# Kernel tuning notes

Hardware: AMD Instinct MI355X
Metric: run time of the kernel (lower is better)

The kernel has to match this reference:

```python
import jax, jax.numpy as jnp
import numpy as np

N_NODES = 100000
D_IN = 128
D_OUT = 128
N_EDGES = 1600000
BN_EPS = 1e-5
LEAKY_SLOPE = 0.01


def setup_inputs() -> dict:
    key = jax.random.key(0)
    ks = jax.random.split(key, 8)
    x = jax.random.normal(ks[0], (N_NODES, D_IN), dtype=jnp.float32)
    edge_index = jax.random.randint(ks[1], (2, N_EDGES), 0, N_NODES, dtype=jnp.int32)
    scale = 1.0 / np.sqrt(D_IN)
    W = jax.random.uniform(ks[2], (D_IN, D_OUT), jnp.float32, -scale, scale)
    b = jax.random.uniform(ks[3], (D_OUT,), jnp.float32, -scale, scale)
    bn_gamma = jnp.ones((D_IN,), jnp.float32)
    bn_beta = jnp.zeros((D_IN,), jnp.float32)
    bn_mean = jax.random.normal(ks[4], (D_IN,), jnp.float32) * 0.01
    bn_var = jax.random.uniform(ks[5], (D_IN,), jnp.float32, 0.5, 1.5)
    rs_W = jax.random.uniform(ks[6], (D_IN, D_OUT), jnp.float32, -scale, scale)
    rs_b = jax.random.uniform(ks[7], (D_OUT,), jnp.float32, -scale, scale)
    return {"x": x, "edge_index": edge_index, "W": W, "b": b,
            "bn_gamma": bn_gamma, "bn_beta": bn_beta,
            "bn_mean": bn_mean, "bn_var": bn_var,
            "rs_W": rs_W, "rs_b": rs_b}


def reference(x, edge_index, W, b, bn_gamma, bn_beta, bn_mean, bn_var, rs_W, rs_b):
    N = x.shape[0]
    # F.normalize: row-wise L2 normalization (eps=1e-12)
    nrm = jnp.sqrt(jnp.sum(x * x, axis=1, keepdims=True))
    x = x / jnp.maximum(nrm, 1e-12)
    # BatchNorm1d (eval mode, running stats)
    x = (x - bn_mean) * jax.lax.rsqrt(bn_var + BN_EPS) * bn_gamma + bn_beta
    # GCNConv: add self-loops, symmetric normalization
    loops = jnp.arange(N, dtype=edge_index.dtype)
    src = jnp.concatenate([edge_index[0], loops])  # [E+N] source j
    dst = jnp.concatenate([edge_index[1], loops])  # [E+N] target i
    deg = jax.ops.segment_sum(jnp.ones(dst.shape, x.dtype), dst, num_segments=N)
    dinv = jax.lax.rsqrt(deg)  # self-loops guarantee deg >= 1
    norm = dinv[src] * dinv[dst]  # [E+N]
    xw = x @ W  # [N, D_OUT]
    msgs = xw[src] * norm[:, None]  # [E+N, D_OUT] gather
    out = jax.ops.segment_sum(msgs, dst, num_segments=N) + b  # scatter-add
    # residual linear on the normalized+BN'd input
    out = out + x @ rs_W + rs_b
    # LeakyReLU (dropout is identity in eval mode)
    return jnp.where(out >= 0, out, LEAKY_SLOPE * out)
```

## Files before the change

kernel.cpp:

```cpp
#include <hip/hip_runtime.h>
#include <hip/hip_fp16.h>


#define NN 100000
#define DD 128
#define EE 1600000
#define BN_EPS 1e-5f
#define SLOPE 0.01f

#define NBKT 98
#define BWID 1024
#define CAPP 20480
#define EPB  4096
#define EBLK 391

struct __align__(8) H4 { __half2 a, b; };

typedef _Float16 f16x8 __attribute__((ext_vector_type(8)));
typedef float    f32x4 __attribute__((ext_vector_type(4)));

__global__ __launch_bounds__(256) void k_binA(const int* __restrict__ src,
                                              const int* __restrict__ dst,
                                              int* __restrict__ gcur,
                                              int* __restrict__ pairs,
                                              const float* __restrict__ W,
                                              const float* __restrict__ rsW,
                                              const float* __restrict__ b,
                                              const float* __restrict__ rb,
                                              __half* __restrict__ WhT,
                                              float* __restrict__ bias2) {
  int t = threadIdx.x;
  if (blockIdx.x >= EBLK) {
    int blk = blockIdx.x - EBLK;
    if (blk == 128) {
      if (t < DD) bias2[t] = b[t] + rb[t];
    } else {
      float v = (t < 128) ? W[t * 128 + blk] : rsW[(t - 128) * 128 + blk];
      WhT[blk * 256 + t] = __float2half(v);
    }
    return;
  }
  __shared__ int hist[2][NBKT];
  __shared__ int cur[2][NBKT];
  int w2 = (t >> 6) & 1;
  if (t < NBKT) { hist[0][t] = 0; hist[1][t] = 0; }
  __syncthreads();
  int e0 = blockIdx.x * EPB;
  #pragma unroll 4
  for (int i = 0; i < EPB / 256; ++i) {
    int e = e0 + i * 256 + t;
    if (e < EE) atomicAdd(&hist[w2][dst[e] >> 10], 1);
  }
  __syncthreads();
  if (t < NBKT) {
    int h0 = hist[0][t], h1 = hist[1][t];
    int b0 = atomicAdd(&gcur[t], h0 + h1);
    cur[0][t] = b0;
    cur[1][t] = b0 + h0;
  }
  __syncthreads();
  #pragma unroll 4
  for (int i = 0; i < EPB / 256; ++i) {
    int e = e0 + i * 256 + t;
    if (e < EE) {
      int d = dst[e], s = src[e];
      int bk = d >> 10;
      int r = atomicAdd(&cur[w2][bk], 1);
      pairs[(size_t)bk * CAPP + r] = ((d & 1023) << 17) | s;
    }
  }
}

__global__ __launch_bounds__(1024) void k_binB(const int* __restrict__ gcur,
                                               const int* __restrict__ pairs,
                                               int* __restrict__ csr,
                                               int2* __restrict__ startdeg,
                                               float* __restrict__ dinv) {
  __shared__ int hist[BWID];
  __shared__ int excl[BWID];
  __shared__ int wsum[16];
  int b = blockIdx.x, t = threadIdx.x;
  hist[t] = 0;
  __syncthreads();
  int pbase = b * CAPP;
  int cnt = gcur[b];
  for (int i = t; i < cnt; i += BWID)
    atomicAdd(&hist[pairs[pbase + i] >> 17], 1);
  __syncthreads();
  int v = hist[t];
  int lane = t & 63, w = t >> 6;
  int incl = v;
  #pragma unroll
  for (int off = 1; off < 64; off <<= 1) {
    int n = __shfl_up(incl, off, 64);
    if (lane >= off) incl += n;
  }
  if (lane == 63) wsum[w] = incl;
  __syncthreads();
  if (t < 16) {
    int orig = wsum[t];
    int s = orig;
    #pragma unroll
    for (int off = 1; off < 16; off <<= 1) {
      int n = __shfl_up(s, off, 64);
      if (t >= off) s += n;
    }
    wsum[t] = s - orig;
  }
  __syncthreads();
  int myexcl = (incl - v) + wsum[w];
  excl[t] = myexcl;
  int node = b * BWID + t;
  if (node < NN) {
    dinv[node] = rsqrtf((float)(v + 1));
    startdeg[node] = make_int2(pbase + myexcl, v);
  }
  __syncthreads();
  for (int i = t; i < cnt; i += BWID) {
    int p = pairs[pbase + i];
    int pos = atomicAdd(&excl[p >> 17], 1);
    csr[pbase + pos] = p & 0x1FFFF;
  }
}

__global__ void k_norm_bn(const float* __restrict__ x,
                          const float* __restrict__ gamma,
                          const float* __restrict__ beta,
                          const float* __restrict__ mean,
                          const float* __restrict__ var,
                          const float* __restrict__ dinv,
                          __half* __restrict__ Ah, __half* __restrict__ zp) {
  int row = blockIdx.x * 4 + (threadIdx.x >> 6);
  int lane = threadIdx.x & 63;
  if (row >= NN) return;
  float2 v = ((const float2*)(x + (size_t)row * DD))[lane];
  float ss = v.x * v.x + v.y * v.y;
  #pragma unroll
  for (int off = 32; off > 0; off >>= 1) ss += __shfl_xor(ss, off);
  float s = 1.0f / fmaxf(sqrtf(ss), 1e-12f);
  float di = dinv[row];
  int c = lane * 2;
  float g0 = gamma[c]     * rsqrtf(var[c]     + BN_EPS);
  float g1 = gamma[c + 1] * rsqrtf(var[c + 1] + BN_EPS);
  float ox = (v.x * s - mean[c])     * g0 + beta[c];
  float oy = (v.y * s - mean[c + 1]) * g1 + beta[c + 1];
  ((__half2*)(Ah + (size_t)row * 256 + 128))[lane] = __floats2half2_rn(ox, oy);
  ((__half2*)(zp + (size_t)row * DD))[lane] = __floats2half2_rn(di * ox, di * oy);
}

__global__ void k_aggregate(const __half* __restrict__ zp,
                            __half* __restrict__ Ah,
                            const int2* __restrict__ startdeg,
                            const int* __restrict__ csr,
                            const float* __restrict__ dinv) {
  int lane = threadIdx.x & 63;
  int half = lane >> 5;
  int l32  = lane & 31;
  int node = blockIdx.x * 8 + (threadIdx.x >> 6) * 2 + half;
  int2 sd = startdeg[node];
  int k = sd.x, end = sd.x + sd.y;
  float di = dinv[node];
  const H4* zr = (const H4*)zp;
  float4 acc = make_float4(0.f, 0.f, 0.f, 0.f);
  for (; k + 8 <= end; k += 8) {
    int j[8];
    #pragma unroll
    for (int u = 0; u < 8; ++u) j[u] = csr[k + u];
    H4 a[8];
    #pragma unroll
    for (int u = 0; u < 8; ++u) a[u] = zr[(size_t)j[u] * 32 + l32];
    #pragma unroll
    for (int u = 0; u < 8; ++u) {
      float2 fa = __half22float2(a[u].a), fb = __half22float2(a[u].b);
      acc.x += fa.x; acc.y += fa.y; acc.z += fb.x; acc.w += fb.y;
    }
  }
  if (k + 4 <= end) {
    int j[4];
    #pragma unroll
    for (int u = 0; u < 4; ++u) j[u] = csr[k + u];
    H4 a[4];
    #pragma unroll
    for (int u = 0; u < 4; ++u) a[u] = zr[(size_t)j[u] * 32 + l32];
    #pragma unroll
    for (int u = 0; u < 4; ++u) {
      float2 fa = __half22float2(a[u].a), fb = __half22float2(a[u].b);
      acc.x += fa.x; acc.y += fa.y; acc.z += fb.x; acc.w += fb.y;
    }
    k += 4;
  }
  for (; k < end; ++k) {
    int j0 = csr[k];
    H4 a0 = zr[(size_t)j0 * 32 + l32];
    float2 fa = __half22float2(a0.a), fb = __half22float2(a0.b);
    acc.x += fa.x; acc.y += fa.y; acc.z += fb.x; acc.w += fb.y;
  }
  H4 zs = zr[(size_t)node * 32 + l32];
  float2 za = __half22float2(zs.a), zb2 = __half22float2(zs.b);
  H4 o;
  o.a = __floats2half2_rn((acc.x + za.x) * di, (acc.y + za.y) * di);
  o.b = __floats2half2_rn((acc.z + zb2.x) * di, (acc.w + zb2.y) * di);
  ((H4*)Ah)[(size_t)node * 64 + l32] = o;
}

__global__ __launch_bounds__(512, 2) void k_gemm(
    const __half* __restrict__ Ah, const __half* __restrict__ WhT,
    const float* __restrict__ bias2, float* __restrict__ out) {
  __shared__ __align__(16) char Bs[65536];
  const int tid = threadIdx.x;
  const int w  = tid >> 6;
  const int l  = tid & 63;
  const int lm = l & 15;
  const int lk = l >> 4;
  const int row0 = blockIdx.x * 256 + w * 32;

  int rA0 = row0 + lm;
  int rA1 = row0 + 16 + lm;
  if (rA0 >= NN) rA0 = NN - 1;
  if (rA1 >= NN) rA1 = NN - 1;

  const __half* a0p = Ah + (size_t)rA0 * 256 + lk * 8;
  const __half* a1p = Ah + (size_t)rA1 * 256 + lk * 8;
  f16x8 a0[8], a1[8];
  #pragma unroll
  for (int ks = 0; ks < 8; ++ks) {
    a0[ks] = *(const f16x8*)(a0p + ks * 32);
    a1[ks] = *(const f16x8*)(a1p + ks * 32);
  }

  #pragma unroll
  for (int i = 0; i < 8; ++i) {
    int idx = tid + i * 512;
    int byte = idx * 16;
    int swz = byte ^ (((byte >> 9) & 7) << 4);
    *(float4*)(Bs + swz) = ((const float4*)WhT)[idx];
  }
  __syncthreads();

  f32x4 acc0[8], acc1[8];
  #pragma unroll
  for (int c = 0; c < 8; ++c) {
    acc0[c] = (f32x4)(0.f);
    acc1[c] = (f32x4)(0.f);
  }

  #pragma unroll
  for (int ks = 0; ks < 8; ++ks) {
    #pragma unroll
    for (int c = 0; c < 8; ++c) {
      int byte = (c * 16 + lm) * 512 + lk * 16 + ks * 64;
      f16x8 b = *(const f16x8*)(Bs + (byte ^ ((lm & 7) << 4)));
      acc0[c] = __builtin_amdgcn_mfma_f32_16x16x32_f16(a0[ks], b, acc0[c], 0, 0, 0);
      acc1[c] = __builtin_amdgcn_mfma_f32_16x16x32_f16(a1[ks], b, acc1[c], 0, 0, 0);
    }
  }

  int orow0 = row0 + lk * 4;
  int orow1 = row0 + 16 + lk * 4;
  #pragma unroll
  for (int c = 0; c < 8; ++c) {
    int col = c * 16 + lm;
    float bs = bias2[col];
    #pragma unroll
    for (int r = 0; r < 4; ++r) {
      int g0 = orow0 + r;
      if (g0 < NN) {
        float v = acc0[c][r] + bs;
        out[(size_t)g0 * 128 + col] = (v >= 0.f) ? v : SLOPE * v;
      }
      int g1 = orow1 + r;
      if (g1 < NN) {
        float v = acc1[c][r] + bs;
        out[(size_t)g1 * 128 + col] = (v >= 0.f) ? v : SLOPE * v;
      }
    }
  }
}

extern "C" void kernel_launch(void* const* d_in, const int* in_sizes, int n_in,
                              void* d_out, int out_size, void* d_ws, size_t ws_size,
                              hipStream_t stream) {
  const float* x     = (const float*)d_in[0];
  const int*   ei    = (const int*)d_in[1];
  const float* W     = (const float*)d_in[2];
  const float* b     = (const float*)d_in[3];
  const float* gamma = (const float*)d_in[4];
  const float* beta  = (const float*)d_in[5];
  const float* mean  = (const float*)d_in[6];
  const float* var   = (const float*)d_in[7];
  const float* rsW   = (const float*)d_in[8];
  const float* rsb   = (const float*)d_in[9];
  float* out = (float*)d_out;
  const int* src = ei;
  const int* dst = ei + EE;

  __half* Ah       = (__half*)d_ws;
  __half* zp       = Ah + (size_t)NN * 256;
  int2*   startdeg = (int2*)(zp + (size_t)NN * DD);
  float*  dinv     = (float*)(startdeg + NN);
  int*    gcur     = (int*)(dinv + NN);
  int*    pairs    = gcur + 128;
  int*    csr      = pairs + NBKT * CAPP;
  __half* WhT      = (__half*)(csr + NBKT * CAPP);
  float*  bias2    = (float*)(WhT + 128 * 256);

  hipMemsetAsync(gcur, 0, 128 * sizeof(int), stream);
  k_binA<<<EBLK + 129, 256, 0, stream>>>(src, dst, gcur, pairs,
                                         W, rsW, b, rsb, WhT, bias2);
  k_binB<<<NBKT, 1024, 0, stream>>>(gcur, pairs, csr, startdeg, dinv);
  k_norm_bn<<<NN / 4, 256, 0, stream>>>(x, gamma, beta, mean, var, dinv, Ah, zp);
  k_aggregate<<<NN / 8, 256, 0, stream>>>(zp, Ah, startdeg, csr, dinv);
  k_gemm<<<(NN + 255) / 256, 512, 0, stream>>>(Ah, WhT, bias2, out);
}
```

Before: 272.6 us.

## Stage binning through LDS, widen aggregate gathers to 16B, shrink GEMM blocks

The first binning pass now sorts each block's edges by bucket in shared memory before writing them out, so global stores become contiguous runs instead of scattered atomically-placed writes. The second pass builds the per-bucket CSR in shared memory and writes it out linearly. Aggregation uses 16 lanes per node with 16-byte f16x8 loads, so each wave handles four nodes. The GEMM drops to 256-thread blocks of 128 rows, so the shared-memory weight tile is loaded more often in total. The new LCAP clamp silently truncates any bucket with more than 18432 edges, which risks wrong results on denser inputs.

```diff
diff --git a/kernel.cpp b/kernel.cpp
--- a/kernel.cpp
+++ b/kernel.cpp
@@ -11,10 +11,9 @@
 #define NBKT 98
 #define BWID 1024
 #define CAPP 20480
+#define LCAP 18432
 #define EPB  4096
 #define EBLK 391
-
-struct __align__(8) H4 { __half2 a, b; };
 
 typedef _Float16 f16x8 __attribute__((ext_vector_type(8)));
 typedef float    f32x4 __attribute__((ext_vector_type(4)));
@@ -40,34 +39,60 @@
     }
     return;
   }
-  __shared__ int hist[2][NBKT];
-  __shared__ int cur[2][NBKT];
-  int w2 = (t >> 6) & 1;
-  if (t < NBKT) { hist[0][t] = 0; hist[1][t] = 0; }
+  __shared__ int hist[NBKT];
+  __shared__ int cur[NBKT];
+  __shared__ int gofs[NBKT];
+  __shared__ int wtot;
+  __shared__ int sortedp[EPB];
+  __shared__ unsigned char sbk[EPB];
+  if (t < NBKT) hist[t] = 0;
   __syncthreads();
   int e0 = blockIdx.x * EPB;
-  #pragma unroll 4
-  for (int i = 0; i < EPB / 256; ++i) {
+  int pr[16];
+  int bkr[16];
+  #pragma unroll
+  for (int i = 0; i < 16; ++i) {
     int e = e0 + i * 256 + t;
-    if (e < EE) atomicAdd(&hist[w2][dst[e] >> 10], 1);
-  }
-  __syncthreads();
-  if (t < NBKT) {
-    int h0 = hist[0][t], h1 = hist[1][t];
-    int b0 = atomicAdd(&gcur[t], h0 + h1);
-    cur[0][t] = b0;
-    cur[1][t] = b0 + h0;
-  }
-  __syncthreads();
-  #pragma unroll 4
-  for (int i = 0; i < EPB / 256; ++i) {
-    int e = e0 + i * 256 + t;
+    bkr[i] = -1;
     if (e < EE) {
       int d = dst[e], s = src[e];
-      int bk = d >> 10;
-      int r = atomicAdd(&cur[w2][bk], 1);
-      pairs[(size_t)bk * CAPP + r] = ((d & 1023) << 17) | s;
-    }
+      bkr[i] = d >> 10;
+      pr[i] = ((d & 1023) << 17) | s;
+      atomicAdd(&hist[bkr[i]], 1);
+    }
+  }
+  __syncthreads();
+  {
+    int v = (t < NBKT) ? hist[t] : 0;
+    int incl = v;
+    #pragma unroll
+    for (int off = 1; off < 64; off <<= 1) {
+      int n = __shfl_up(incl, off, 64);
+      if ((t & 63) >= off) incl += n;
+    }
+    if (t == 63) wtot = incl;
+    __syncthreads();
+    if (t < NBKT) {
+      int ex = incl - v + ((t >= 64) ? wtot : 0);
+      cur[t] = ex;
+      int gb = atomicAdd(&gcur[t], v);
+      gofs[t] = t * CAPP + gb - ex;
+    }
+  }
+  __syncthreads();
+  #pragma unroll
+  for (int i = 0; i < 16; ++i) {
+    if (bkr[i] >= 0) {
+      int r = atomicAdd(&cur[bkr[i]], 1);
+      sortedp[r] = pr[i];
+      sbk[r] = (unsigned char)bkr[i];
+    }
+  }
+  __syncthreads();
+  int cnt = min(EPB, EE - e0);
+  for (int i = t; i < cnt; i += 256) {
+    int bq = sbk[i];
+    pairs[gofs[bq] + i] = sortedp[i];
   }
 }
 
@@ -79,11 +104,13 @@
   __shared__ int hist[BWID];
   __shared__ int excl[BWID];
   __shared__ int wsum[16];
+  __shared__ int sortedp[LCAP];
   int b = blockIdx.x, t = threadIdx.x;
   hist[t] = 0;
   __syncthreads();
   int pbase = b * CAPP;
   int cnt = gcur[b];
+  if (cnt > LCAP) cnt = LCAP;
   for (int i = t; i < cnt; i += BWID)
     atomicAdd(&hist[pairs[pbase + i] >> 17], 1);
   __syncthreads();
@@ -119,8 +146,11 @@
   for (int i = t; i < cnt; i += BWID) {
     int p = pairs[pbase + i];
     int pos = atomicAdd(&excl[p >> 17], 1);
-    csr[pbase + pos] = p & 0x1FFFF;
-  }
+    sortedp[pos] = p & 0x1FFFF;
+  }
+  __syncthreads();
+  for (int i = t; i < cnt; i += BWID)
+    csr[pbase + i] = sortedp[i];
 }
 
 __global__ void k_norm_bn(const float* __restrict__ x,
@@ -154,56 +184,54 @@
                             const int* __restrict__ csr,
                             const float* __restrict__ dinv) {
   int lane = threadIdx.x & 63;
-  int half = lane >> 5;
-  int l32  = lane & 31;
-  int node = blockIdx.x * 8 + (threadIdx.x >> 6) * 2 + half;
+  int q   = lane >> 4;
+  int l16 = lane & 15;
+  int node = blockIdx.x * 16 + (threadIdx.x >> 6) * 4 + q;
   int2 sd = startdeg[node];
   int k = sd.x, end = sd.x + sd.y;
   float di = dinv[node];
-  const H4* zr = (const H4*)zp;
-  float4 acc = make_float4(0.f, 0.f, 0.f, 0.f);
+  const f16x8* zr = (const f16x8*)zp;
+  float acc[8] = {0.f, 0.f, 0.f, 0.f, 0.f, 0.f, 0.f, 0.f};
   for (; k + 8 <= end; k += 8) {
     int j[8];
     #pragma unroll
     for (int u = 0; u < 8; ++u) j[u] = csr[k + u];
-    H4 a[8];
-    #pragma unroll
-    for (int u = 0; u < 8; ++u) a[u] = zr[(size_t)j[u] * 32 + l32];
-    #pragma unroll
-    for (int u = 0; u < 8; ++u) {
-      float2 fa = __half22float2(a[u].a), fb = __half22float2(a[u].b);
-      acc.x += fa.x; acc.y += fa.y; acc.z += fb.x; acc.w += fb.y;
-    }
+    f16x8 a[8];
+    #pragma unroll
+    for (int u = 0; u < 8; ++u) a[u] = zr[(size_t)j[u] * 16 + l16];
+    #pragma unroll
+    for (int u = 0; u < 8; ++u)
+      #pragma unroll
+      for (int vv = 0; vv < 8; ++vv) acc[vv] += (float)a[u][vv];
   }
   if (k + 4 <= end) {
     int j[4];
     #pragma unroll
     for (int u = 0; u < 4; ++u) j[u] = csr[k + u];
-    H4 a[4];
-    #pragma unroll
-    for (int u = 0; u < 4; ++u) a[u] = zr[(size_t)j[u] * 32 + l32];
-    #pragma unroll
-    for (int u = 0; u < 4; ++u) {
-      float2 fa = __half22float2(a[u].a), fb = __half22float2(a[u].b);
-      acc.x += fa.x; acc.y += fa.y; acc.z += fb.x; acc.w += fb.y;
-    }
+    f16x8 a[4];
+    #pragma unroll
+    for (int u = 0; u < 4; ++u) a[u] = zr[(size_t)j[u] * 16 + l16];
+    #pragma unroll
+    for (int u = 0; u < 4; ++u)
+      #pragma unroll
+      for (int vv = 0; vv < 8; ++vv) acc[vv] += (float)a[u][vv];
     k += 4;
   }
   for (; k < end; ++k) {
     int j0 = csr[k];
-    H4 a0 = zr[(size_t)j0 * 32 + l32];
-    float2 fa = __half22float2(a0.a), fb = __half22float2(a0.b);
-    acc.x += fa.x; acc.y += fa.y; acc.z += fb.x; acc.w += fb.y;
-  }
-  H4 zs = zr[(size_t)node * 32 + l32];
-  float2 za = __half22float2(zs.a), zb2 = __half22float2(zs.b);
-  H4 o;
-  o.a = __floats2half2_rn((acc.x + za.x) * di, (acc.y + za.y) * di);
-  o.b = __floats2half2_rn((acc.z + zb2.x) * di, (acc.w + zb2.y) * di);
-  ((H4*)Ah)[(size_t)node * 64 + l32] = o;
-}
-
-__global__ __launch_bounds__(512, 2) void k_gemm(
+    f16x8 a0 = zr[(size_t)j0 * 16 + l16];
+    #pragma unroll
+    for (int vv = 0; vv < 8; ++vv) acc[vv] += (float)a0[vv];
+  }
+  f16x8 zs = zr[(size_t)node * 16 + l16];
+  f16x8 o;
+  #pragma unroll
+  for (int vv = 0; vv < 8; ++vv)
+    o[vv] = (_Float16)((acc[vv] + (float)zs[vv]) * di);
+  ((f16x8*)Ah)[(size_t)node * 32 + l16] = o;
+}
+
+__global__ __launch_bounds__(256) void k_gemm(
     const __half* __restrict__ Ah, const __half* __restrict__ WhT,
     const float* __restrict__ bias2, float* __restrict__ out) {
   __shared__ __align__(16) char Bs[65536];
@@ -212,7 +240,7 @@
   const int l  = tid & 63;
   const int lm = l & 15;
   const int lk = l >> 4;
-  const int row0 = blockIdx.x * 256 + w * 32;
+  const int row0 = blockIdx.x * 128 + w * 32;
 
   int rA0 = row0 + lm;
   int rA1 = row0 + 16 + lm;
@@ -229,8 +257,8 @@
   }
 
   #pragma unroll
-  for (int i = 0; i < 8; ++i) {
-    int idx = tid + i * 512;
+  for (int i = 0; i < 16; ++i) {
+    int idx = tid + i * 256;
     int byte = idx * 16;
     int swz = byte ^ (((byte >> 9) & 7) << 4);
     *(float4*)(Bs + swz) = ((const float4*)WhT)[idx];
@@ -309,6 +337,6 @@
                                          W, rsW, b, rsb, WhT, bias2);
   k_binB<<<NBKT, 1024, 0, stream>>>(gcur, pairs, csr, startdeg, dinv);
   k_norm_bn<<<NN / 4, 256, 0, stream>>>(x, gamma, beta, mean, var, dinv, Ah, zp);
-  k_aggregate<<<NN / 8, 256, 0, stream>>>(zp, Ah, startdeg, csr, dinv);
-  k_gemm<<<(NN + 255) / 256, 512, 0, stream>>>(Ah, WhT, bias2, out);
-}
+  k_aggregate<<<NN / 16, 256, 0, stream>>>(zp, Ah, startdeg, csr, dinv);
+  k_gemm<<<(NN + 127) / 128, 256, 0, stream>>>(Ah, WhT, bias2, out);
+}
```

Result: faster. 257.0 us (-5.7%).
